# Optimization experiments

Measured on AMD Instinct MI355X. Metric: run time of the kernel, lower is better.

Reference implementation:

```python
import jax, jax.numpy as jnp
import numpy as np

B, N_LR, N_HR = 2, 8192, 16384
C = 32          # feature channels (query_ch = neigh_ch = 32 in Grouper7)
NSAMPLE = 64    # nsamples=[64]
RADIUS = 1.0    # radius=[1.0]
LR_VOX = np.array([0.4, 0.4, 1.0], np.float32)   # lr_voxel_size (x,y,z)
HR_VOX = np.array([0.05, 0.05, 0.1], np.float32) # hr_voxel_size (x,y,z)
OFFSET = np.array([0.0, -40.0, -3.0], np.float32)


def setup_inputs() -> dict:
    key = jax.random.key(0)
    ks = jax.random.split(key, 6)
    lr_idx = jax.random.randint(ks[0], (B, N_LR, 3), 0, 25, dtype=jnp.int32)    # (z,y,x) voxel coords
    hr_idx = jax.random.randint(ks[1], (B, N_HR, 3), 0, 200, dtype=jnp.int32)
    lr_feat = jax.random.normal(ks[2], (B, N_LR, C), jnp.float32)
    hr_feat = jax.random.normal(ks[3], (B, N_HR, C), jnp.float32)
    # Grouper7 MLP [[32,32]] on use_xyz-augmented neighbor feats (3+C -> 32 -> 32), bn=False
    W1 = jax.random.normal(ks[4], (C + 3, C), jnp.float32) * 0.1
    b1 = jnp.zeros((C,), jnp.float32)
    W2 = jax.random.normal(ks[5], (C, C), jnp.float32) * 0.1
    b2 = jnp.zeros((C,), jnp.float32)
    return dict(lr_idx=lr_idx, hr_idx=hr_idx, lr_feat=lr_feat, hr_feat=hr_feat,
                W1=W1, b1=b1, W2=W2, b2=b2)


def _to_xyz(idx, vox, off):
    # spconv indices are (z,y,x); code does indices[:, [3,2,1]] * voxel_size + offset + 0.5*voxel_size
    return idx[..., ::-1].astype(jnp.float32) * vox + off + 0.5 * vox


def _group_one(lr_xyz, hr_xyz, hr_f, W1, b1, W2, b2):
    # ball query: first NSAMPLE hr points within RADIUS of each lr query point
    d2 = jnp.sum((lr_xyz[:, None, :] - hr_xyz[None, :, :]) ** 2, axis=-1)  # [N_lr, N_hr]
    mask = d2 <= RADIUS ** 2
    order = jnp.where(mask, -jnp.arange(hr_xyz.shape[0], dtype=jnp.float32), -jnp.inf)
    _, idx = jax.lax.top_k(order, NSAMPLE)            # lowest valid indices first (PointNet++ semantics)
    valid = jnp.take_along_axis(mask, idx, axis=1)
    first = jnp.where(valid[:, :1], idx[:, :1], 0)
    idx = jnp.where(valid, idx, first)                # pad empty slots with first valid neighbor (0 if none)
    rel = hr_xyz[idx] - lr_xyz[:, None, :]            # [N_lr, ns, 3] relative coords (use_xyz=True)
    g = jnp.concatenate([rel, hr_f[idx]], axis=-1)    # [N_lr, ns, 3+C]
    h = jax.nn.relu(g @ W1 + b1)                      # shared 1x1-conv MLP, bn=False
    h = jax.nn.relu(h @ W2 + b2)
    return h.max(axis=1)                              # max-pool over neighbors -> [N_lr, C]


def reference(lr_idx, hr_idx, lr_feat, hr_feat, W1, b1, W2, b2):
    vox_lr = jnp.asarray(LR_VOX)
    vox_hr = jnp.asarray(HR_VOX)
    off = jnp.asarray(OFFSET)
    lr_xyz = _to_xyz(lr_idx, vox_lr, off)             # [B, N_lr, 3]
    hr_xyz = _to_xyz(hr_idx, vox_hr, off)             # [B, N_hr, 3]
    new = jax.vmap(_group_one, in_axes=(0, 0, 0, None, None, None, None))(
        lr_xyz, hr_xyz, hr_feat, W1, b1, W2, b2)      # [B, N_lr, C]
    # structured_forward: torch.cat([lr_features, new_lr_features], dim=-1)
    return jnp.concatenate([lr_feat, new], axis=-1)   # [B, N_lr, 2C]
```

## Files before the change

kernel.cpp:

```cpp
#include <hip/hip_runtime.h>
#include <hip/hip_bf16.h>
#include <cstdint>
#include <cstddef>
#include <climits>

constexpr int B_   = 2;
constexpr int NLR  = 8192;
constexpr int NHR  = 16384;
constexpr int CCH  = 32;
constexpr int NS   = 64;
constexpr int THREADS = 256;

constexpr int GX = 11, GY = 11, GZ = 20;
constexpr int NCELLS = GX * GY * GZ;
constexpr int NCT    = B_ * NCELLS;
constexpr int CAP    = 192;
constexpr float SCALE = 0.999f;

typedef __attribute__((ext_vector_type(8))) short bf16x8;
typedef __attribute__((ext_vector_type(4))) float f32x4;

__device__ __forceinline__ float cvt_coord(int i, float vox, float off) {
    return __fadd_rn(__fadd_rn(__fmul_rn((float)i, vox), off), __fmul_rn(0.5f, vox));
}

__device__ __forceinline__ void hr_coords(const int* ip, float& x, float& y, float& z) {
    x = cvt_coord(ip[2], 0.05f,   0.0f);
    y = cvt_coord(ip[1], 0.05f, -40.0f);
    z = cvt_coord(ip[0], 0.1f,   -3.0f);
}

__device__ __forceinline__ int cell_of(float x, float y, float z) {
    const int cx = (int)(__fmul_rn(x, SCALE));
    const int cy = (int)(__fmul_rn(__fadd_rn(y, 40.0f), SCALE));
    const int cz = (int)(__fmul_rn(__fadd_rn(z,  3.0f), SCALE));
    return (cz * GY + cy) * GX + cx;
}

__device__ __forceinline__ unsigned short f2bf(float f) {
    __hip_bfloat16 h = __float2bfloat16(f);
    return __builtin_bit_cast(unsigned short, h);
}

extern "C" __global__ void k_hist(const int* __restrict__ hr_idx, int* __restrict__ cnt) {
    const int gid = blockIdx.x * THREADS + threadIdx.x;
    const int b = gid >> 14;
    const int* ip = hr_idx + (size_t)gid * 3;
    float x, y, z;
    hr_coords(ip, x, y, z);
    atomicAdd(&cnt[b * NCELLS + cell_of(x, y, z)], 1);
}

extern "C" __global__ void k_scan(const int* __restrict__ cnt, int* __restrict__ start,
                                  int* __restrict__ cursor) {
    __shared__ int sums[THREADS];
    constexpr int CH = (NCT + THREADS - 1) / THREADS;
    const int t = threadIdx.x;
    int loc[CH];
    int s = 0;
#pragma unroll
    for (int k = 0; k < CH; ++k) {
        const int i = t * CH + k;
        loc[k] = s;
        s += (i < NCT) ? cnt[i] : 0;
    }
    sums[t] = s;
    __syncthreads();
    for (int off = 1; off < THREADS; off <<= 1) {
        const int v = (t >= off) ? sums[t - off] : 0;
        __syncthreads();
        sums[t] += v;
        __syncthreads();
    }
    const int pre = (t > 0) ? sums[t - 1] : 0;
#pragma unroll
    for (int k = 0; k < CH; ++k) {
        const int i = t * CH + k;
        if (i < NCT) {
            const int st = pre + loc[k];
            start[i]  = st;
            cursor[i] = st;
        }
    }
    if (t == THREADS - 1) start[NCT] = sums[THREADS - 1];
}

extern "C" __global__ void k_scatter(const int* __restrict__ hr_idx, int* __restrict__ cursor,
                                     float4* __restrict__ pts) {
    const int gid = blockIdx.x * THREADS + threadIdx.x;
    const int b = gid >> 14;
    const int i = gid & (NHR - 1);
    const int* ip = hr_idx + (size_t)gid * 3;
    float x, y, z;
    hr_coords(ip, x, y, z);
    const int c = b * NCELLS + cell_of(x, y, z);
    const int slot = atomicAdd(&cursor[c], 1);
    float4 v;
    v.x = x; v.y = y; v.z = z; v.w = __int_as_float(i);
    pts[slot] = v;
}

extern "C" __global__ void __launch_bounds__(THREADS)
k_group(const int* __restrict__ lr_idx, const int* __restrict__ hr_idx,
        const float* __restrict__ lr_feat, const float* __restrict__ hr_feat,
        const float* __restrict__ W1, const float* __restrict__ b1,
        const float* __restrict__ W2, const float* __restrict__ b2,
        const int* __restrict__ start, const float4* __restrict__ pts,
        float* __restrict__ out)
{
    __shared__ __align__(16) unsigned short W1f[2][2][64][8];
    __shared__ __align__(16) unsigned short W2f[2][64][8];
    __shared__ __align__(16) unsigned short Xf[4][64][32];
    __shared__ __align__(16) unsigned short XYZ[4][64][4];
    __shared__ __align__(16) unsigned short Hb[4][64][32];
    __shared__ int cand[4][CAP];

    const int tid  = threadIdx.x;
    const int wave = tid >> 6;
    const int lane = tid & 63;
    const int q    = blockIdx.x * 4 + wave;
    const int b    = q >> 13;

#pragma unroll
    for (int e = 0; e < 8; ++e) {
        const int flat = tid * 8 + e;
        const int j  = flat & 7;
        const int l  = (flat >> 3) & 63;
        const int ct = (flat >> 9) & 1;
        const int ks = (flat >> 10) & 1;
        const int kp = ks * 32 + (l >> 4) * 8 + j;
        const int n  = ct * 16 + (l & 15);
        float v = 0.0f;
        if (kp < 32)       v = W1[(kp + 3) * 32 + n];
        else if (kp < 35)  v = W1[(kp - 32) * 32 + n];
        W1f[ks][ct][l][j] = f2bf(v);
    }
#pragma unroll
    for (int e = 0; e < 4; ++e) {
        const int flat = tid * 4 + e;
        const int j  = flat & 7;
        const int l  = (flat >> 3) & 63;
        const int ct = (flat >> 9) & 1;
        const int k  = (l >> 4) * 8 + j;
        const int n  = ct * 16 + (l & 15);
        W2f[ct][l][j] = f2bf(W2[k * 32 + n]);
    }
    __syncthreads();

    const int* qip = lr_idx + (size_t)q * 3;
    const float qx = cvt_coord(qip[2], 0.4f,   0.0f);
    const float qy = cvt_coord(qip[1], 0.4f, -40.0f);
    const float qz = cvt_coord(qip[0], 1.0f,  -3.0f);

    const int cqx = (int)(__fmul_rn(qx, SCALE));
    const int cqy = (int)(__fmul_rn(__fadd_rn(qy, 40.0f), SCALE));
    const int cqz = (int)(__fmul_rn(__fadd_rn(qz,  3.0f), SCALE));
    const int x0 = max(cqx - 1, 0), x1 = min(cqx + 1, GX - 1);
    const int y0 = max(cqy - 1, 0), y1 = min(cqy + 1, GY - 1);
    const int z0 = max(cqz - 1, 0), z1 = min(cqz + 1, GZ - 1);
    const int nx = x1 - x0 + 1;
    const int bbase = b * NCELLS;

    int cnt = 0;
    for (int zz = z0; zz <= z1; ++zz)
    for (int yy = y0; yy <= y1; ++yy) {
        const int g0 = bbase + (zz * GY + yy) * GX + x0;
        const int s  = start[g0];
        const int e  = start[g0 + nx];
        for (int base = s; base < e; base += 64) {
            const int j = base + lane;
            bool ok = false;
            int id = 0;
            if (j < e) {
                const float4 pv = pts[j];
                const float dx = __fsub_rn(qx, pv.x);
                const float dy = __fsub_rn(qy, pv.y);
                const float dz = __fsub_rn(qz, pv.z);
                const float d2 = __fadd_rn(__fadd_rn(__fmul_rn(dx, dx),
                                                     __fmul_rn(dy, dy)),
                                           __fmul_rn(dz, dz));
                ok = d2 <= 1.0f;
                id = __float_as_int(pv.w);
            }
            const unsigned long long m = __ballot(ok);
            if (m != 0ull) {
                const int before = (int)__popcll(m & ((1ull << lane) - 1ull));
                const int pos = cnt + before;
                if (ok && pos < CAP) cand[wave][pos] = id;
                cnt += (int)__popcll(m);
                if (cnt > CAP) cnt = CAP;
            }
        }
    }

    int pid;
    if (cnt <= NS) {
        int myid = (lane < cnt) ? cand[wave][lane] : INT_MAX;
        int mp = myid;
#pragma unroll
        for (int s = 32; s >= 1; s >>= 1) mp = min(mp, __shfl_xor(mp, s, 64));
        pid = (lane < cnt) ? myid : ((cnt > 0) ? mp : 0);
    } else {
        const int c = cnt;
        int mine = 0;
        for (int k = 0; k < NS; ++k) {
            int lm = INT_MAX;
            for (int j = lane; j < c; j += 64) lm = min(lm, cand[wave][j]);
#pragma unroll
            for (int s = 32; s >= 1; s >>= 1) lm = min(lm, __shfl_xor(lm, s, 64));
            for (int j = lane; j < c; j += 64)
                if (cand[wave][j] == lm) cand[wave][j] = INT_MAX;
            if (lane == k) mine = lm;
        }
        pid = mine;
    }

    {
        const int* ip = hr_idx + ((size_t)b * NHR + pid) * 3;
        float px, py, pz;
        hr_coords(ip, px, py, pz);
        const int r = lane;
        ushort4 t;
        t.x = f2bf(__fsub_rn(px, qx));
        t.y = f2bf(__fsub_rn(py, qy));
        t.z = f2bf(__fsub_rn(pz, qz));
        t.w = 0;
        *reinterpret_cast<ushort4*>(&XYZ[wave][r][0]) = t;
        const float4* fp = reinterpret_cast<const float4*>(hr_feat + ((size_t)b * NHR + pid) * CCH);
#pragma unroll
        for (int c = 0; c < 4; ++c) {
            const float4 a = fp[2 * c];
            const float4 d = fp[2 * c + 1];
            uint4 u;
            u.x = (unsigned)f2bf(a.x) | ((unsigned)f2bf(a.y) << 16);
            u.y = (unsigned)f2bf(a.z) | ((unsigned)f2bf(a.w) << 16);
            u.z = (unsigned)f2bf(d.x) | ((unsigned)f2bf(d.y) << 16);
            u.w = (unsigned)f2bf(d.z) | ((unsigned)f2bf(d.w) << 16);
            const int byteoff = (c * 16) ^ ((r & 3) << 4);
            *reinterpret_cast<uint4*>(reinterpret_cast<char*>(&Xf[wave][r][0]) + byteoff) = u;
        }
    }

    const int hi  = lane >> 4;
    const int c15 = lane & 15;

    bf16x8 B1[2][2];
#pragma unroll
    for (int ks = 0; ks < 2; ++ks)
#pragma unroll
        for (int ct = 0; ct < 2; ++ct)
            B1[ks][ct] = *reinterpret_cast<const bf16x8*>(&W1f[ks][ct][lane][0]);

    const f32x4 zero4 = {0.0f, 0.0f, 0.0f, 0.0f};
    f32x4 acc[4][2];
#pragma unroll
    for (int rt = 0; rt < 4; ++rt) { acc[rt][0] = zero4; acc[rt][1] = zero4; }

#pragma unroll
    for (int rt = 0; rt < 4; ++rt) {
        const int row = rt * 16 + c15;
        const int byteoff = (hi * 16) ^ ((row & 3) << 4);
        const bf16x8 a0 = *reinterpret_cast<const bf16x8*>(
            reinterpret_cast<const char*>(&Xf[wave][row][0]) + byteoff);
        bf16x8 a1 = {0, 0, 0, 0, 0, 0, 0, 0};
        if (hi == 0) {
            const ushort4 t = *reinterpret_cast<const ushort4*>(&XYZ[wave][row][0]);
            a1[0] = (short)t.x; a1[1] = (short)t.y; a1[2] = (short)t.z;
        }
#pragma unroll
        for (int ct = 0; ct < 2; ++ct) {
            acc[rt][ct] = __builtin_amdgcn_mfma_f32_16x16x32_bf16(a0, B1[0][ct], acc[rt][ct], 0, 0, 0);
            acc[rt][ct] = __builtin_amdgcn_mfma_f32_16x16x32_bf16(a1, B1[1][ct], acc[rt][ct], 0, 0, 0);
        }
    }

    const float bias1_0 = b1[c15];
    const float bias1_1 = b1[16 + c15];
#pragma unroll
    for (int rt = 0; rt < 4; ++rt)
#pragma unroll
        for (int ct = 0; ct < 2; ++ct) {
            const float bb = ct ? bias1_1 : bias1_0;
#pragma unroll
            for (int rr = 0; rr < 4; ++rr) {
                const float v = fmaxf(acc[rt][ct][rr] + bb, 0.0f);
                const int row = rt * 16 + hi * 4 + rr;
                const int boff = (ct * 32 + c15 * 2) ^ ((row & 3) << 4);
                *reinterpret_cast<unsigned short*>(
                    reinterpret_cast<char*>(&Hb[wave][row][0]) + boff) = f2bf(v);
            }
        }

    bf16x8 B2[2];
#pragma unroll
    for (int ct = 0; ct < 2; ++ct)
        B2[ct] = *reinterpret_cast<const bf16x8*>(&W2f[ct][lane][0]);

    f32x4 acc2[4][2];
#pragma unroll
    for (int rt = 0; rt < 4; ++rt) { acc2[rt][0] = zero4; acc2[rt][1] = zero4; }

#pragma unroll
    for (int rt = 0; rt < 4; ++rt) {
        const int row = rt * 16 + c15;
        const int byteoff = (hi * 16) ^ ((row & 3) << 4);
        const bf16x8 a = *reinterpret_cast<const bf16x8*>(
            reinterpret_cast<const char*>(&Hb[wave][row][0]) + byteoff);
#pragma unroll
        for (int ct = 0; ct < 2; ++ct)
            acc2[rt][ct] = __builtin_amdgcn_mfma_f32_16x16x32_bf16(a, B2[ct], acc2[rt][ct], 0, 0, 0);
    }

    const float bias2_0 = b2[c15];
    const float bias2_1 = b2[16 + c15];
    float m0 = 0.0f, m1 = 0.0f;
#pragma unroll
    for (int rt = 0; rt < 4; ++rt)
#pragma unroll
        for (int rr = 0; rr < 4; ++rr) {
            m0 = fmaxf(m0, fmaxf(acc2[rt][0][rr] + bias2_0, 0.0f));
            m1 = fmaxf(m1, fmaxf(acc2[rt][1][rr] + bias2_1, 0.0f));
        }
    m0 = fmaxf(m0, __shfl_xor(m0, 16, 64));
    m0 = fmaxf(m0, __shfl_xor(m0, 32, 64));
    m1 = fmaxf(m1, __shfl_xor(m1, 16, 64));
    m1 = fmaxf(m1, __shfl_xor(m1, 32, 64));

    float* orow = out + (size_t)q * (2 * CCH);
    if (lane < CCH)
        orow[lane] = lr_feat[(size_t)q * CCH + lane];
    if (lane < 16) {
        orow[CCH + lane]      = m0;
        orow[CCH + 16 + lane] = m1;
    }
}

extern "C" void kernel_launch(void* const* d_in, const int* in_sizes, int n_in,
                              void* d_out, int out_size, void* d_ws, size_t ws_size,
                              hipStream_t stream) {
    const int*   lr_idx  = (const int*)  d_in[0];
    const int*   hr_idx  = (const int*)  d_in[1];
    const float* lr_feat = (const float*)d_in[2];
    const float* hr_feat = (const float*)d_in[3];
    const float* W1      = (const float*)d_in[4];
    const float* b1      = (const float*)d_in[5];
    const float* W2      = (const float*)d_in[6];
    const float* b2      = (const float*)d_in[7];
    float* out = (float*)d_out;

    int*    cell_count  = (int*)d_ws;
    int*    cell_start  = cell_count + NCT;
    int*    cell_cursor = cell_start + (NCT + 1);
    size_t  off = ((size_t)(3 * NCT + 1) * sizeof(int) + 15) & ~(size_t)15;
    float4* pts = (float4*)((char*)d_ws + off);

    hipMemsetAsync(cell_count, 0, NCT * sizeof(int), stream);

    const dim3 blk(THREADS);
    hipLaunchKernelGGL(k_hist,    dim3(B_ * NHR / THREADS), blk, 0, stream, hr_idx, cell_count);
    hipLaunchKernelGGL(k_scan,    dim3(1),                  blk, 0, stream, cell_count, cell_start, cell_cursor);
    hipLaunchKernelGGL(k_scatter, dim3(B_ * NHR / THREADS), blk, 0, stream, hr_idx, cell_cursor, pts);
    hipLaunchKernelGGL(k_group,   dim3(B_ * NLR / 4),       blk, 0, stream,
                       lr_idx, hr_idx, lr_feat, hr_feat, W1, b1, W2, b2,
                       cell_start, pts, out);
}
```

Before: 149.5 us.

## Fuse grid histogram, scan and scatter into one single-block build kernel

Replaces the memset plus three separate launches (histogram, scan, scatter) with a single 1024-thread block that builds the cell histogram in shared memory, scans it, and scatters points using shared-memory cursors. This removes launch and global-atomic overhead for the spatial binning. The trade-off is that all 32K points are handled by one block on a single CU. The group kernel also reuses one shared buffer for both the input features and the hidden activations, cutting its LDS footprint, which may raise occupancy.

```diff
diff --git a/kernel.cpp b/kernel.cpp
--- a/kernel.cpp
+++ b/kernel.cpp
@@ -10,6 +10,7 @@
 constexpr int CCH  = 32;
 constexpr int NS   = 64;
 constexpr int THREADS = 256;
+constexpr int BT   = 1024;
 
 constexpr int GX = 11, GY = 11, GZ = 20;
 constexpr int NCELLS = GX * GY * GZ;
@@ -42,31 +43,44 @@
     return __builtin_bit_cast(unsigned short, h);
 }
 
-extern "C" __global__ void k_hist(const int* __restrict__ hr_idx, int* __restrict__ cnt) {
-    const int gid = blockIdx.x * THREADS + threadIdx.x;
-    const int b = gid >> 14;
-    const int* ip = hr_idx + (size_t)gid * 3;
-    float x, y, z;
-    hr_coords(ip, x, y, z);
-    atomicAdd(&cnt[b * NCELLS + cell_of(x, y, z)], 1);
-}
-
-extern "C" __global__ void k_scan(const int* __restrict__ cnt, int* __restrict__ start,
-                                  int* __restrict__ cursor) {
-    __shared__ int sums[THREADS];
-    constexpr int CH = (NCT + THREADS - 1) / THREADS;
+extern "C" __global__ void __launch_bounds__(BT)
+k_build(const int* __restrict__ hr_idx, int* __restrict__ start,
+        float4* __restrict__ pts)
+{
+    __shared__ int hist[NCT];
+    __shared__ int sums[BT];
     const int t = threadIdx.x;
+
+    for (int i = t; i < NCT; i += BT) hist[i] = 0;
+    __syncthreads();
+
+    constexpr int PPT = B_ * NHR / BT;
+    int cellv[PPT];
+#pragma unroll
+    for (int it = 0; it < PPT; ++it) {
+        const int gid = it * BT + t;
+        const int bb  = gid >> 14;
+        const int* ip = hr_idx + (size_t)gid * 3;
+        float x, y, z;
+        hr_coords(ip, x, y, z);
+        const int c = bb * NCELLS + cell_of(x, y, z);
+        cellv[it] = c;
+        atomicAdd(&hist[c], 1);
+    }
+    __syncthreads();
+
+    constexpr int CH = (NCT + BT - 1) / BT;
     int loc[CH];
     int s = 0;
 #pragma unroll
     for (int k = 0; k < CH; ++k) {
         const int i = t * CH + k;
         loc[k] = s;
-        s += (i < NCT) ? cnt[i] : 0;
+        s += (i < NCT) ? hist[i] : 0;
     }
     sums[t] = s;
     __syncthreads();
-    for (int off = 1; off < THREADS; off <<= 1) {
+    for (int off = 1; off < BT; off <<= 1) {
         const int v = (t >= off) ? sums[t - off] : 0;
         __syncthreads();
         sums[t] += v;
@@ -78,26 +92,24 @@
         const int i = t * CH + k;
         if (i < NCT) {
             const int st = pre + loc[k];
-            start[i]  = st;
-            cursor[i] = st;
-        }
-    }
-    if (t == THREADS - 1) start[NCT] = sums[THREADS - 1];
-}
-
-extern "C" __global__ void k_scatter(const int* __restrict__ hr_idx, int* __restrict__ cursor,
-                                     float4* __restrict__ pts) {
-    const int gid = blockIdx.x * THREADS + threadIdx.x;
-    const int b = gid >> 14;
-    const int i = gid & (NHR - 1);
-    const int* ip = hr_idx + (size_t)gid * 3;
-    float x, y, z;
-    hr_coords(ip, x, y, z);
-    const int c = b * NCELLS + cell_of(x, y, z);
-    const int slot = atomicAdd(&cursor[c], 1);
-    float4 v;
-    v.x = x; v.y = y; v.z = z; v.w = __int_as_float(i);
-    pts[slot] = v;
+            start[i] = st;
+            hist[i]  = st;
+        }
+    }
+    if (t == BT - 1) start[NCT] = sums[BT - 1];
+    __syncthreads();
+
+#pragma unroll
+    for (int it = 0; it < PPT; ++it) {
+        const int gid = it * BT + t;
+        const int* ip = hr_idx + (size_t)gid * 3;
+        float x, y, z;
+        hr_coords(ip, x, y, z);
+        const int slot = atomicAdd(&hist[cellv[it]], 1);
+        float4 v;
+        v.x = x; v.y = y; v.z = z; v.w = __int_as_float(gid & (NHR - 1));
+        pts[slot] = v;
+    }
 }
 
 extern "C" __global__ void __launch_bounds__(THREADS)
@@ -110,9 +122,8 @@
 {
     __shared__ __align__(16) unsigned short W1f[2][2][64][8];
     __shared__ __align__(16) unsigned short W2f[2][64][8];
-    __shared__ __align__(16) unsigned short Xf[4][64][32];
+    __shared__ __align__(16) unsigned short XH[4][64][32];
     __shared__ __align__(16) unsigned short XYZ[4][64][4];
-    __shared__ __align__(16) unsigned short Hb[4][64][32];
     __shared__ int cand[4][CAP];
 
     const int tid  = threadIdx.x;
@@ -237,7 +248,7 @@
             u.z = (unsigned)f2bf(d.x) | ((unsigned)f2bf(d.y) << 16);
             u.w = (unsigned)f2bf(d.z) | ((unsigned)f2bf(d.w) << 16);
             const int byteoff = (c * 16) ^ ((r & 3) << 4);
-            *reinterpret_cast<uint4*>(reinterpret_cast<char*>(&Xf[wave][r][0]) + byteoff) = u;
+            *reinterpret_cast<uint4*>(reinterpret_cast<char*>(&XH[wave][r][0]) + byteoff) = u;
         }
     }
 
@@ -261,7 +272,7 @@
         const int row = rt * 16 + c15;
         const int byteoff = (hi * 16) ^ ((row & 3) << 4);
         const bf16x8 a0 = *reinterpret_cast<const bf16x8*>(
-            reinterpret_cast<const char*>(&Xf[wave][row][0]) + byteoff);
+            reinterpret_cast<const char*>(&XH[wave][row][0]) + byteoff);
         bf16x8 a1 = {0, 0, 0, 0, 0, 0, 0, 0};
         if (hi == 0) {
             const ushort4 t = *reinterpret_cast<const ushort4*>(&XYZ[wave][row][0]);
@@ -287,7 +298,7 @@
                 const int row = rt * 16 + hi * 4 + rr;
                 const int boff = (ct * 32 + c15 * 2) ^ ((row & 3) << 4);
                 *reinterpret_cast<unsigned short*>(
-                    reinterpret_cast<char*>(&Hb[wave][row][0]) + boff) = f2bf(v);
+                    reinterpret_cast<char*>(&XH[wave][row][0]) + boff) = f2bf(v);
             }
         }
 
@@ -305,7 +316,7 @@
         const int row = rt * 16 + c15;
         const int byteoff = (hi * 16) ^ ((row & 3) << 4);
         const bf16x8 a = *reinterpret_cast<const bf16x8*>(
-            reinterpret_cast<const char*>(&Hb[wave][row][0]) + byteoff);
+            reinterpret_cast<const char*>(&XH[wave][row][0]) + byteoff);
 #pragma unroll
         for (int ct = 0; ct < 2; ++ct)
             acc2[rt][ct] = __builtin_amdgcn_mfma_f32_16x16x32_bf16(a, B2[ct], acc2[rt][ct], 0, 0, 0);
@@ -348,19 +359,13 @@
     const float* b2      = (const float*)d_in[7];
     float* out = (float*)d_out;
 
-    int*    cell_count  = (int*)d_ws;
-    int*    cell_start  = cell_count + NCT;
-    int*    cell_cursor = cell_start + (NCT + 1);
-    size_t  off = ((size_t)(3 * NCT + 1) * sizeof(int) + 15) & ~(size_t)15;
+    int*    cell_start = (int*)d_ws;
+    size_t  off = ((size_t)(NCT + 1) * sizeof(int) + 15) & ~(size_t)15;
     float4* pts = (float4*)((char*)d_ws + off);
 
-    hipMemsetAsync(cell_count, 0, NCT * sizeof(int), stream);
-
-    const dim3 blk(THREADS);
-    hipLaunchKernelGGL(k_hist,    dim3(B_ * NHR / THREADS), blk, 0, stream, hr_idx, cell_count);
-    hipLaunchKernelGGL(k_scan,    dim3(1),                  blk, 0, stream, cell_count, cell_start, cell_cursor);
-    hipLaunchKernelGGL(k_scatter, dim3(B_ * NHR / THREADS), blk, 0, stream, hr_idx, cell_cursor, pts);
-    hipLaunchKernelGGL(k_group,   dim3(B_ * NLR / 4),       blk, 0, stream,
+    hipLaunchKernelGGL(k_build, dim3(1),             dim3(BT),      0, stream,
+                       hr_idx, cell_start, pts);
+    hipLaunchKernelGGL(k_group, dim3(B_ * NLR / 4),  dim3(THREADS), 0, stream,
                        lr_idx, hr_idx, lr_feat, hr_feat, W1, b1, W2, b2,
                        cell_start, pts, out);
 }
```

Result: slower. 165.3 us (+10.6%).
